# Optimization experiments

Hardware: AMD Instinct MI355X
Metric: run time of the kernel (lower is better)

Reference implementation:

```python
import jax, jax.numpy as jnp
import numpy as np

NUM_SINK = 20        # num_iterations
LAMBD = 0.002        # entropy_weight
B, M, N = 64, 512, 512


def setup_inputs() -> dict:
    key = jax.random.key(0)
    k1, k2, k3 = jax.random.split(key, 3)
    c = jax.random.uniform(k1, (B, M, N), dtype=jnp.float32)
    # positive marginals, bounded away from zero so log() is finite
    a = jax.random.uniform(k2, (B, M), dtype=jnp.float32, minval=0.5, maxval=1.5)
    b = jax.random.uniform(k3, (B, N), dtype=jnp.float32, minval=0.5, maxval=1.5)
    return {"c": c, "a": a, "b": b}


def reference(c, a, b):
    """Log-domain Sinkhorn: returns soft transport plan p = exp(log_p), shape [B,M,N]."""
    log_a = jnp.log(a)[..., :, None]   # [B,M,1]
    log_b = jnp.log(b)[..., None, :]   # [B,1,N]
    log_p0 = -c / LAMBD

    def body(log_p, _):
        # column normalization then row normalization, both in log domain
        log_p = log_p - (jax.scipy.special.logsumexp(log_p, axis=-2, keepdims=True) - log_b)
        log_p = log_p - (jax.scipy.special.logsumexp(log_p, axis=-1, keepdims=True) - log_a)
        return log_p, None

    log_p, _ = jax.lax.scan(body, log_p0, None, length=NUM_SINK)
    return jnp.exp(log_p)
```

## Files before the change

kernel.cpp:

```cpp
#include <hip/hip_runtime.h>

#define BB 64
#define MM 512
#define NN 512
#define NUM_SINK 20
#define SLICES 4

constexpr float NEG_K2 = -(1.4426950408889634f / 0.002f);

__device__ __forceinline__ float exp2fast(float x) { return __builtin_amdgcn_exp2f(x); }
__device__ __forceinline__ float log2fast(float x) { return __builtin_amdgcn_logf(x); }
__device__ __forceinline__ float rcpfast(float x)  { return __builtin_amdgcn_rcpf(x); }

typedef unsigned long long u64;
typedef unsigned u32;

__device__ __forceinline__ void st_tag(u64* p, float v, u32 tag) {
    u64 x = ((u64)tag << 32) | (u64)__float_as_uint(v);
    __hip_atomic_store(p, x, __ATOMIC_RELAXED, __HIP_MEMORY_SCOPE_AGENT);
}
__device__ __forceinline__ u64 ld_tag(const u64* p) {
    return __hip_atomic_load(p, __ATOMIC_RELAXED, __HIP_MEMORY_SCOPE_AGENT);
}

__device__ __forceinline__ void barrier_lds() {
    asm volatile("s_waitcnt lgkmcnt(0)" ::: "memory");
    __builtin_amdgcn_s_barrier();
    asm volatile("" ::: "memory");
    __builtin_amdgcn_sched_barrier(0);
}

__global__ __launch_bounds__(1024, 4) void sink_flow5(
    const float* __restrict__ c, const float* __restrict__ amarg,
    const float* __restrict__ bmarg, float* __restrict__ out,
    u64* __restrict__ colTag)
{
    __shared__ float sPartial[16][NN];
    __shared__ float sV[NN];

    const int wg    = blockIdx.x;
    const int b     = (wg & 7) * 8 + (wg >> 5);
    const int slice = (wg >> 3) & 3;
    const int t     = threadIdx.x;
    const int wave  = t >> 6;
    const int lane  = t & 63;

    const int mrow  = slice * 128 + wave * 8;
    const float* cw = c   + (size_t)b * MM * NN + (size_t)mrow * NN + lane * 4;
    float*       ow = out + (size_t)b * MM * NN + (size_t)mrow * NN + lane * 4;
    const size_t PBUF = (size_t)BB * SLICES * NN;
    u64* tb         = colTag + (size_t)b * SLICES * NN;

    const float bT = (t < NN) ? bmarg[b * NN + t] : 0.f;
    float aw[8];
    #pragma unroll
    for (int r = 0; r < 8; ++r) aw[r] = amarg[b * MM + mrow + r];

    float k[8][8];
    float ca[8];
    #pragma unroll
    for (int j = 0; j < 8; ++j) ca[j] = 0.f;
    #pragma unroll
    for (int r = 0; r < 8; ++r) {
        const float4 c0 = *(const float4*)(cw + (size_t)r * NN);
        const float4 c1 = *(const float4*)(cw + (size_t)r * NN + 256);
        k[r][0] = exp2fast(c0.x * NEG_K2);  k[r][1] = exp2fast(c0.y * NEG_K2);
        k[r][2] = exp2fast(c0.z * NEG_K2);  k[r][3] = exp2fast(c0.w * NEG_K2);
        k[r][4] = exp2fast(c1.x * NEG_K2);  k[r][5] = exp2fast(c1.y * NEG_K2);
        k[r][6] = exp2fast(c1.z * NEG_K2);  k[r][7] = exp2fast(c1.w * NEG_K2);
        #pragma unroll
        for (int j = 0; j < 8; ++j) ca[j] += k[r][j];
    }
    *(float4*)&sPartial[wave][lane * 4]       = make_float4(ca[0], ca[1], ca[2], ca[3]);
    *(float4*)&sPartial[wave][lane * 4 + 256] = make_float4(ca[4], ca[5], ca[6], ca[7]);
    __syncthreads();
    if (t < NN) {
        float p16 = 0.f;
        #pragma unroll
        for (int w = 0; w < 16; ++w) p16 += sPartial[w][t];
        st_tag(&tb[slice * NN + t], p16, 1u);
    }

    float vold = 1.0f;
    for (int j = 1; j <= NUM_SINK; ++j) {
        const u64* rb = colTag + (size_t)((j - 1) & 1) * PBUF + (size_t)b * SLICES * NN;
        u64*       wb = colTag + (size_t)(j & 1) * PBUF       + (size_t)b * SLICES * NN;
        const u32  etag = (u32)j;

        if (t < NN) {
            const u64* p0 = &rb[0 * NN + t];
            const u64* p1 = &rb[1 * NN + t];
            const u64* p2 = &rb[2 * NN + t];
            const u64* p3 = &rb[3 * NN + t];
            u64 x0, x1, x2, x3;
            for (;;) {
                x0 = ld_tag(p0); x1 = ld_tag(p1);
                x2 = ld_tag(p2); x3 = ld_tag(p3);
                const bool ok = ((u32)(x0 >> 32) == etag) & ((u32)(x1 >> 32) == etag)
                              & ((u32)(x2 >> 32) == etag) & ((u32)(x3 >> 32) == etag);
                if (ok) break;
                __builtin_amdgcn_s_sleep(1);
            }
            const float s4 = __uint_as_float((u32)x0) + __uint_as_float((u32)x1)
                           + __uint_as_float((u32)x2) + __uint_as_float((u32)x3);
            const float v = bT * vold * rcpfast(s4);
            vold = v;
            sV[t] = v;
        }
        barrier_lds();

        const float4 v0 = *(const float4*)&sV[lane * 4];
        const float4 v1 = *(const float4*)&sV[lane * 4 + 256];
        const bool  last = (j == NUM_SINK);

        #pragma unroll
        for (int i = 0; i < 8; ++i) ca[i] = 0.f;

        #pragma unroll
        for (int r = 0; r < 8; ++r) {
            const float e0 = k[r][0] * v0.x, e1 = k[r][1] * v0.y;
            const float e2 = k[r][2] * v0.z, e3 = k[r][3] * v0.w;
            const float e4 = k[r][4] * v1.x, e5 = k[r][5] * v1.y;
            const float e6 = k[r][6] * v1.z, e7 = k[r][7] * v1.w;
            float s = ((e0 + e1) + (e2 + e3)) + ((e4 + e5) + (e6 + e7));
            #pragma unroll
            for (int o = 32; o > 0; o >>= 1) s += __shfl_xor(s, o, 64);
            const float ts = aw[r] * rcpfast(s);

            if (!last) {
                ca[0] = fmaf(ts, e0, ca[0]);  ca[1] = fmaf(ts, e1, ca[1]);
                ca[2] = fmaf(ts, e2, ca[2]);  ca[3] = fmaf(ts, e3, ca[3]);
                ca[4] = fmaf(ts, e4, ca[4]);  ca[5] = fmaf(ts, e5, ca[5]);
                ca[6] = fmaf(ts, e6, ca[6]);  ca[7] = fmaf(ts, e7, ca[7]);
            } else {
                *(float4*)(ow + (size_t)r * NN)       =
                    make_float4(ts * e0, ts * e1, ts * e2, ts * e3);
                *(float4*)(ow + (size_t)r * NN + 256) =
                    make_float4(ts * e4, ts * e5, ts * e6, ts * e7);
            }
        }

        if (!last) {
            *(float4*)&sPartial[wave][lane * 4]       = make_float4(ca[0], ca[1], ca[2], ca[3]);
            *(float4*)&sPartial[wave][lane * 4 + 256] = make_float4(ca[4], ca[5], ca[6], ca[7]);
            barrier_lds();
            if (t < NN) {
                float p16 = 0.f;
                #pragma unroll
                for (int w = 0; w < 16; ++w) p16 += sPartial[w][t];
                st_tag(&wb[slice * NN + t], p16, (u32)(j + 1));
            }
        }
    }
}

__device__ __forceinline__ float block_max512(float v, float* sRed) {
    const int t = threadIdx.x;
    float wm = v;
    #pragma unroll
    for (int o = 32; o > 0; o >>= 1) wm = fmaxf(wm, __shfl_xor(wm, o, 64));
    if ((t & 63) == 0) sRed[t >> 6] = wm;
    __syncthreads();
    if (t == 0) {
        float m2 = sRed[0];
        #pragma unroll
        for (int i = 1; i < 8; ++i) m2 = fmaxf(m2, sRed[i]);
        sRed[0] = m2;
    }
    __syncthreads();
    const float r = sRed[0];
    __syncthreads();
    return r;
}

__global__ __launch_bounds__(512) void col_kernel(
    const float* __restrict__ c, const float* __restrict__ bmarg,
    const float* __restrict__ F, float* __restrict__ G, int first)
{
    __shared__ float sF[MM];
    __shared__ float sPart[16][128];
    __shared__ float sRed[8];

    const int b  = blockIdx.x >> 2;
    const int n0 = (blockIdx.x & 3) * 128;
    const int t  = threadIdx.x;

    float maxF = 0.0f, v = 0.0f;
    if (!first) {
        v = F[b * MM + t];
        maxF = block_max512(v, sRed);
    }
    sF[t] = v - maxF;
    __syncthreads();

    const int lane_c = t & 31;
    const int mg     = t >> 5;
    const int n4     = n0 + lane_c * 4;
    const float* cp  = c + (size_t)b * MM * NN;
    const int m0     = mg * 32;

    float s0 = 0.f, s1 = 0.f, s2 = 0.f, s3 = 0.f;
    #pragma unroll 4
    for (int r = 0; r < 32; ++r) {
        const int m = m0 + r;
        const float fp = sF[m];
        const float4 cv = *(const float4*)(cp + (size_t)m * NN + n4);
        s0 += exp2fast(fmaf(cv.x, NEG_K2, fp));
        s1 += exp2fast(fmaf(cv.y, NEG_K2, fp));
        s2 += exp2fast(fmaf(cv.z, NEG_K2, fp));
        s3 += exp2fast(fmaf(cv.w, NEG_K2, fp));
    }
    sPart[mg][lane_c * 4 + 0] = s0;
    sPart[mg][lane_c * 4 + 1] = s1;
    sPart[mg][lane_c * 4 + 2] = s2;
    sPart[mg][lane_c * 4 + 3] = s3;
    __syncthreads();

    if (t < 128) {
        float tot = 0.f;
        #pragma unroll
        for (int g = 0; g < 16; ++g) tot += sPart[g][t];
        const int n = n0 + t;
        G[b * NN + n] = log2fast(bmarg[b * NN + n]) - maxF - log2fast(tot);
    }
}

template <bool WRITE_OUT>
__global__ __launch_bounds__(512) void row_kernel(
    const float* __restrict__ c, const float* __restrict__ amarg,
    const float* __restrict__ G, float* __restrict__ F, float* __restrict__ out)
{
    __shared__ float sG2[NN];
    __shared__ float sRed[8];

    const int b  = blockIdx.x >> 3;
    const int m0 = (blockIdx.x & 7) * 64;
    const int t  = threadIdx.x;

    const float v    = G[b * NN + t];
    const float maxG = block_max512(v, sRed);
    sG2[t] = v - maxG;
    __syncthreads();

    const int wave = t >> 6;
    const int lane = t & 63;
    const float* cp = c + (size_t)b * MM * NN;

    const float4 g0 = *(const float4*)&sG2[lane * 4];
    const float4 g1 = *(const float4*)&sG2[lane * 4 + 256];

    #pragma unroll 2
    for (int r = 0; r < 8; ++r) {
        const int m = m0 + wave * 8 + r;
        const float* rowp = cp + (size_t)m * NN;
        const float4 c0 = *(const float4*)(rowp + lane * 4);
        const float4 c1 = *(const float4*)(rowp + lane * 4 + 256);

        float s = exp2fast(fmaf(c0.x, NEG_K2, g0.x)) + exp2fast(fmaf(c0.y, NEG_K2, g0.y))
                + exp2fast(fmaf(c0.z, NEG_K2, g0.z)) + exp2fast(fmaf(c0.w, NEG_K2, g0.w))
                + exp2fast(fmaf(c1.x, NEG_K2, g1.x)) + exp2fast(fmaf(c1.y, NEG_K2, g1.y))
                + exp2fast(fmaf(c1.z, NEG_K2, g1.z)) + exp2fast(fmaf(c1.w, NEG_K2, g1.w));
        #pragma unroll
        for (int o = 32; o > 0; o >>= 1) s += __shfl_xor(s, o, 64);

        const float Fm = log2fast(amarg[b * MM + m]) - maxG - log2fast(s);
        if (lane == 0) F[b * MM + m] = Fm;

        if (WRITE_OUT) {
            const float base = Fm + maxG;
            float4 o0, o1;
            o0.x = exp2fast(fmaf(c0.x, NEG_K2, base + g0.x));
            o0.y = exp2fast(fmaf(c0.y, NEG_K2, base + g0.y));
            o0.z = exp2fast(fmaf(c0.z, NEG_K2, base + g0.z));
            o0.w = exp2fast(fmaf(c0.w, NEG_K2, base + g0.w));
            o1.x = exp2fast(fmaf(c1.x, NEG_K2, base + g1.x));
            o1.y = exp2fast(fmaf(c1.y, NEG_K2, base + g1.y));
            o1.z = exp2fast(fmaf(c1.z, NEG_K2, base + g1.z));
            o1.w = exp2fast(fmaf(c1.w, NEG_K2, base + g1.w));
            float* op = out + (size_t)b * MM * NN + (size_t)m * NN;
            *(float4*)(op + lane * 4)       = o0;
            *(float4*)(op + lane * 4 + 256) = o1;
        }
    }
}

extern "C" void kernel_launch(void* const* d_in, const int* in_sizes, int n_in,
                              void* d_out, int out_size, void* d_ws, size_t ws_size,
                              hipStream_t stream) {
    const float* c  = (const float*)d_in[0];
    const float* am = (const float*)d_in[1];
    const float* bm = (const float*)d_in[2];
    float* out = (float*)d_out;

    const size_t TAGBYTES = 2ull * BB * SLICES * NN * sizeof(u64);

    if (ws_size >= TAGBYTES) {
        u64* colTag = (u64*)d_ws;
        hipMemsetAsync(colTag, 0, TAGBYTES, stream);
        hipLaunchKernelGGL(sink_flow5, dim3(BB * SLICES), dim3(1024), 0, stream,
                           c, am, bm, out, colTag);
    } else {
        float* F = (float*)d_ws;
        float* G = F + BB * MM;
        for (int it = 0; it < NUM_SINK; ++it) {
            hipLaunchKernelGGL(col_kernel, dim3(BB * 4), dim3(512), 0, stream,
                               c, bm, F, G, it == 0 ? 1 : 0);
            if (it < NUM_SINK - 1)
                hipLaunchKernelGGL(row_kernel<false>, dim3(BB * 8), dim3(512), 0, stream,
                                   c, am, G, F, out);
            else
                hipLaunchKernelGGL(row_kernel<true>, dim3(BB * 8), dim3(512), 0, stream,
                                   c, am, G, F, out);
        }
    }
}
```

Baseline: 110.6 us.

## Replace per-element tagged column sums with data buffers and per-slice flags

Cross-workgroup column partial sums were published as 64-bit words that packed a tag with the value, and 512 threads spun on those tags. Now plain float data is written, followed by a block barrier and a single per-slice flag store. On the reader side one thread polls four flags, then a barrier releases the workgroup to load the data. This halves the exchanged bytes and cuts polling traffic. In exchange it adds a serial flag hop and extra block barriers to every iteration. It also relies on relaxed atomics without an explicit release/acquire fence to order the data before the flag.

```diff
diff --git a/kernel.cpp b/kernel.cpp
--- a/kernel.cpp
+++ b/kernel.cpp
@@ -15,11 +15,16 @@
 typedef unsigned long long u64;
 typedef unsigned u32;
 
-__device__ __forceinline__ void st_tag(u64* p, float v, u32 tag) {
-    u64 x = ((u64)tag << 32) | (u64)__float_as_uint(v);
-    __hip_atomic_store(p, x, __ATOMIC_RELAXED, __HIP_MEMORY_SCOPE_AGENT);
-}
-__device__ __forceinline__ u64 ld_tag(const u64* p) {
+__device__ __forceinline__ void st_dat(float* p, float v) {
+    __hip_atomic_store(p, v, __ATOMIC_RELAXED, __HIP_MEMORY_SCOPE_AGENT);
+}
+__device__ __forceinline__ float ld_dat(const float* p) {
+    return __hip_atomic_load(p, __ATOMIC_RELAXED, __HIP_MEMORY_SCOPE_AGENT);
+}
+__device__ __forceinline__ void st_flag(u32* p, u32 v) {
+    __hip_atomic_store(p, v, __ATOMIC_RELAXED, __HIP_MEMORY_SCOPE_AGENT);
+}
+__device__ __forceinline__ u32 ld_flag(const u32* p) {
     return __hip_atomic_load(p, __ATOMIC_RELAXED, __HIP_MEMORY_SCOPE_AGENT);
 }
 
@@ -30,10 +35,11 @@
     __builtin_amdgcn_sched_barrier(0);
 }
 
-__global__ __launch_bounds__(1024, 4) void sink_flow5(
+__global__ __launch_bounds__(1024, 4) void sink_flag(
     const float* __restrict__ c, const float* __restrict__ amarg,
     const float* __restrict__ bmarg, float* __restrict__ out,
-    u64* __restrict__ colTag)
+    float* __restrict__ colDat,
+    u32* __restrict__ flg)
 {
     __shared__ float sPartial[16][NN];
     __shared__ float sV[NN];
@@ -49,7 +55,8 @@
     const float* cw = c   + (size_t)b * MM * NN + (size_t)mrow * NN + lane * 4;
     float*       ow = out + (size_t)b * MM * NN + (size_t)mrow * NN + lane * 4;
     const size_t PBUF = (size_t)BB * SLICES * NN;
-    u64* tb         = colTag + (size_t)b * SLICES * NN;
+    float* db       = colDat + (size_t)b * SLICES * NN;
+    u32*   fb       = flg + b * SLICES;
 
     const float bT = (t < NN) ? bmarg[b * NN + t] : 0.f;
     float aw[8];
@@ -78,31 +85,35 @@
         float p16 = 0.f;
         #pragma unroll
         for (int w = 0; w < 16; ++w) p16 += sPartial[w][t];
-        st_tag(&tb[slice * NN + t], p16, 1u);
-    }
+        st_dat(&db[slice * NN + t], p16);
+    }
+    __syncthreads();
+    if (t == 0) st_flag(&fb[slice], 1u);
 
     float vold = 1.0f;
     for (int j = 1; j <= NUM_SINK; ++j) {
-        const u64* rb = colTag + (size_t)((j - 1) & 1) * PBUF + (size_t)b * SLICES * NN;
-        u64*       wb = colTag + (size_t)(j & 1) * PBUF       + (size_t)b * SLICES * NN;
-        const u32  etag = (u32)j;
-
-        if (t < NN) {
-            const u64* p0 = &rb[0 * NN + t];
-            const u64* p1 = &rb[1 * NN + t];
-            const u64* p2 = &rb[2 * NN + t];
-            const u64* p3 = &rb[3 * NN + t];
-            u64 x0, x1, x2, x3;
+        const float* rb = colDat + (size_t)((j - 1) & 1) * PBUF + (size_t)b * SLICES * NN;
+        float*       wb = colDat + (size_t)(j & 1) * PBUF       + (size_t)b * SLICES * NN;
+        const u32    etag = (u32)j;
+
+        if (t == 0) {
             for (;;) {
-                x0 = ld_tag(p0); x1 = ld_tag(p1);
-                x2 = ld_tag(p2); x3 = ld_tag(p3);
-                const bool ok = ((u32)(x0 >> 32) == etag) & ((u32)(x1 >> 32) == etag)
-                              & ((u32)(x2 >> 32) == etag) & ((u32)(x3 >> 32) == etag);
-                if (ok) break;
+                const u32 f0 = ld_flag(&fb[0]);
+                const u32 f1 = ld_flag(&fb[1]);
+                const u32 f2 = ld_flag(&fb[2]);
+                const u32 f3 = ld_flag(&fb[3]);
+                if (f0 >= etag && f1 >= etag && f2 >= etag && f3 >= etag) break;
                 __builtin_amdgcn_s_sleep(1);
             }
-            const float s4 = __uint_as_float((u32)x0) + __uint_as_float((u32)x1)
-                           + __uint_as_float((u32)x2) + __uint_as_float((u32)x3);
+        }
+        barrier_lds();
+
+        if (t < NN) {
+            const float d0 = ld_dat(&rb[0 * NN + t]);
+            const float d1 = ld_dat(&rb[1 * NN + t]);
+            const float d2 = ld_dat(&rb[2 * NN + t]);
+            const float d3 = ld_dat(&rb[3 * NN + t]);
+            const float s4 = (d0 + d1) + (d2 + d3);
             const float v = bT * vold * rcpfast(s4);
             vold = v;
             sV[t] = v;
@@ -143,13 +154,15 @@
         if (!last) {
             *(float4*)&sPartial[wave][lane * 4]       = make_float4(ca[0], ca[1], ca[2], ca[3]);
             *(float4*)&sPartial[wave][lane * 4 + 256] = make_float4(ca[4], ca[5], ca[6], ca[7]);
-            barrier_lds();
+            __syncthreads();
             if (t < NN) {
                 float p16 = 0.f;
                 #pragma unroll
                 for (int w = 0; w < 16; ++w) p16 += sPartial[w][t];
-                st_tag(&wb[slice * NN + t], p16, (u32)(j + 1));
+                st_dat(&wb[slice * NN + t], p16);
             }
+            __syncthreads();
+            if (t == 0) st_flag(&fb[slice], (u32)(j + 1));
         }
     }
 }
@@ -292,13 +305,15 @@
     const float* bm = (const float*)d_in[2];
     float* out = (float*)d_out;
 
-    const size_t TAGBYTES = 2ull * BB * SLICES * NN * sizeof(u64);
-
-    if (ws_size >= TAGBYTES) {
-        u64* colTag = (u64*)d_ws;
-        hipMemsetAsync(colTag, 0, TAGBYTES, stream);
-        hipLaunchKernelGGL(sink_flow5, dim3(BB * SLICES), dim3(1024), 0, stream,
-                           c, am, bm, out, colTag);
+    const size_t DATBYTES  = 2ull * BB * SLICES * NN * sizeof(float);
+    const size_t FLAGBYTES = (size_t)BB * SLICES * sizeof(u32);
+
+    if (ws_size >= DATBYTES + FLAGBYTES) {
+        float* colDat = (float*)d_ws;
+        u32*   flg    = (u32*)((char*)d_ws + DATBYTES);
+        hipMemsetAsync(d_ws, 0, DATBYTES + FLAGBYTES, stream);
+        hipLaunchKernelGGL(sink_flag, dim3(BB * SLICES), dim3(1024), 0, stream,
+                           c, am, bm, out, colDat, flg);
     } else {
         float* F = (float*)d_ws;
         float* G = F + BB * MM;
```

Measured after the change: 133.4 us. 20.6% more time.
